# Optimization experiments

Hardware: AMD Instinct MI355X
Metric: run time of the kernel (lower is better)

Reference implementation:

```python
import jax, jax.numpy as jnp
import numpy as np

B, C, HH, WW = 8, 512, 32, 32
HEADS, GROUPS, EPS = 8, 32, 1e-5


def setup_inputs() -> dict:
    key = jax.random.key(0)
    k0, k1, k2 = jax.random.split(key, 3)
    x = jax.random.normal(k0, (B, C, HH, WW), jnp.float32)
    gamma = jnp.ones((C,), jnp.float32)
    beta = jnp.zeros((C,), jnp.float32)
    # 1x1 convs modeled as (out, in) matrices; fan-in scaling keeps logits sane
    w_qkv = jax.random.normal(k1, (3 * C, C), jnp.float32) * (C ** -0.5)
    b_qkv = jnp.zeros((3 * C,), jnp.float32)
    w_proj = jax.random.normal(k2, (C, C), jnp.float32) * (C ** -0.5)
    b_proj = jnp.zeros((C,), jnp.float32)
    return {"x": x, "gamma": gamma, "beta": beta, "w_qkv": w_qkv,
            "b_qkv": b_qkv, "w_proj": w_proj, "b_proj": b_proj}


def reference(x, gamma, beta, w_qkv, b_qkv, w_proj, b_proj):
    b, c, h, w = x.shape
    S = h * w
    xr = x.reshape(b, c, S)
    # GroupNorm(32, C) over (channels_in_group, spatial)
    xg = xr.reshape(b, GROUPS, c // GROUPS, S)
    mu = xg.mean(axis=(2, 3), keepdims=True)
    var = xg.var(axis=(2, 3), keepdims=True)
    xn = ((xg - mu) * jax.lax.rsqrt(var + EPS)).reshape(b, c, S)
    xn = xn * gamma[None, :, None] + beta[None, :, None]
    # qkv 1x1 conv: (B, 3C, S)
    qkv = jnp.einsum('oc,bcs->bos', w_qkv, xn) + b_qkv[None, :, None]
    D = c // HEADS
    qkv = qkv.reshape(b, 3, HEADS, D, S)  # channel layout: (three, H, D)
    q = jnp.transpose(qkv[:, 0], (0, 1, 3, 2))  # (B, H, S, D)
    k = jnp.transpose(qkv[:, 1], (0, 1, 3, 2))
    v = jnp.transpose(qkv[:, 2], (0, 1, 3, 2))
    scale = 1.0 / float(np.sqrt(np.sqrt(D)))
    logits = jnp.einsum('bhtd,bhsd->bhts', q * scale, k * scale)  # (B,H,S,S)
    logits = logits - jnp.max(logits, axis=-1, keepdims=True)
    probs = jax.nn.softmax(logits, axis=-1)  # dropout p=0 (default)
    attn = jnp.einsum('bhts,bhsd->bhtd', probs, v)  # (B,H,S,D)
    hout = jnp.transpose(attn, (0, 1, 3, 2)).reshape(b, c, S)  # (B, H*D=C, S)
    hout = jnp.einsum('oc,bcs->bos', w_proj, hout) + b_proj[None, :, None]
    return (hout + xr).reshape(b, c, h, w)
```

## Files before the change

kernel.cpp:

```cpp
#include <hip/hip_runtime.h>
#include <hip/hip_bf16.h>

typedef __hip_bfloat16 bf16;
typedef unsigned short u16;
typedef __attribute__((ext_vector_type(8))) short bf16x8;
typedef __attribute__((ext_vector_type(4))) float f32x4;

static constexpr int Bn = 8;
static constexpr int C = 512;
static constexpr int S = 1024;
static constexpr int NH = 8;
static constexpr int HD = 64;
static constexpr int CPG = 16;
#define EPSV 1e-5f

__device__ __forceinline__ u16 f2bf(float f) {
    bf16 h = __float2bfloat16(f);
    return *reinterpret_cast<u16*>(&h);
}

__device__ __forceinline__ void async_copy16(const void* g, void* l) {
    __builtin_amdgcn_global_load_lds(
        (const __attribute__((address_space(1))) void*)g,
        (__attribute__((address_space(3))) void*)l, 16, 0, 0);
}

__global__ __launch_bounds__(256) void wconv(const float* __restrict__ w,
                                             u16* __restrict__ out) {
    int i = (blockIdx.x * 256 + threadIdx.x) * 4;
    float4 v = *reinterpret_cast<const float4*>(&w[i]);
    float sc = (i < 512 * 512) ? 0.125f : 1.f;
    u16 t[4] = {f2bf(v.x * sc), f2bf(v.y * sc), f2bf(v.z * sc), f2bf(v.w * sc)};
    *reinterpret_cast<uint2*>(&out[i]) = *reinterpret_cast<uint2*>(t);
}

__global__ __launch_bounds__(256) void gn_stats(const float* __restrict__ x,
                                                float* __restrict__ stats) {
    const int tid = threadIdx.x;
    const int bg = blockIdx.x;
    const size_t base = (size_t)bg * CPG * S;
    const int N = CPG * S;
    float sum = 0.f, sq = 0.f;
    for (int i = tid * 4; i < N; i += 1024) {
        float4 v = *reinterpret_cast<const float4*>(&x[base + i]);
        sum += v.x + v.y + v.z + v.w;
        sq += v.x * v.x + v.y * v.y + v.z * v.z + v.w * v.w;
    }
#pragma unroll
    for (int off = 32; off > 0; off >>= 1) {
        sum += __shfl_down(sum, off, 64);
        sq  += __shfl_down(sq,  off, 64);
    }
    __shared__ float s0[4], s1[4];
    if ((tid & 63) == 0) { s0[tid >> 6] = sum; s1[tid >> 6] = sq; }
    __syncthreads();
    if (tid == 0) {
        float a  = s0[0] + s0[1] + s0[2] + s0[3];
        float b2 = s1[0] + s1[1] + s1[2] + s1[3];
        float mu = a / (float)N;
        float var = fmaxf(b2 / (float)N - mu * mu, 0.f);
        stats[bg] = mu;
        stats[256 + bg] = rsqrtf(var + EPSV);
    }
}

__global__ __launch_bounds__(256) void gn_apply_t(const float* __restrict__ x,
                                                  const float* __restrict__ gamma,
                                                  const float* __restrict__ beta,
                                                  const float* __restrict__ stats,
                                                  u16* __restrict__ xnt) {
    const int b = blockIdx.z, c0 = blockIdx.y * 64, s0 = blockIdx.x * 64;
    const int tid = threadIdx.x;
    __shared__ u16 T[64 * 72];
    const float* xb = x + ((size_t)b * C + c0) * S;
#pragma unroll
    for (int i = 0; i < 4; ++i) {
        int ch = i * 256 + tid;
        int c = ch >> 4, seg = ch & 15;
        int cg = c0 + c;
        float mu = stats[b * 32 + (cg >> 4)];
        float rstd = stats[256 + b * 32 + (cg >> 4)];
        float ga = gamma[cg], be = beta[cg];
        float4 v = *reinterpret_cast<const float4*>(&xb[(size_t)c * S + s0 + seg * 4]);
        float vals[4] = {v.x, v.y, v.z, v.w};
#pragma unroll
        for (int j = 0; j < 4; ++j)
            T[(seg * 4 + j) * 72 + c] = f2bf((vals[j] - mu) * rstd * ga + be);
    }
    __syncthreads();
#pragma unroll
    for (int i = 0; i < 2; ++i) {
        int ch = i * 256 + tid;
        int r = ch >> 3, seg = ch & 7;
        uint4 val = *reinterpret_cast<const uint4*>(&T[r * 72 + seg * 8]);
        *reinterpret_cast<uint4*>(&xnt[(size_t)(b * S + s0 + r) * C + c0 + seg * 8]) = val;
    }
}

template <int MODE>
__global__ __launch_bounds__(256) void mfma_gemm(const float* __restrict__ Wf,
                                                 const u16* __restrict__ Wb,
                                                 const u16* __restrict__ Xt,
                                                 const float* __restrict__ bias,
                                                 const float* __restrict__ resid,
                                                 u16* __restrict__ qkvT,
                                                 u16* __restrict__ qkvV,
                                                 float* __restrict__ Yf) {
    const int K = 512;
    const int b = blockIdx.z, o0 = blockIdx.y * 128, s0 = blockIdx.x * 128;
    const int tid = threadIdx.x;
    const int lane = tid & 63, w = tid >> 6;
    const int quad = lane >> 4, l15 = lane & 15;
    const int wr = w >> 1, wc = w & 1;
    __shared__ u16 As[128 * 64];
    __shared__ u16 Bs[128 * 64];
    f32x4 acc[4][4] = {};
    const u16* Xb = Xt + (size_t)(b * S + s0) * K;
    for (int k0 = 0; k0 < K; k0 += 64) {
        if (MODE == 0) {
#pragma unroll
            for (int i = 0; i < 4; ++i) {
                int ci = w * 4 + i;
                int r = ci * 8 + (lane >> 3);
                int c = (lane & 7) ^ (r & 7);
                async_copy16(&Wb[(size_t)(o0 + r) * K + k0 + c * 8], &As[ci * 512]);
            }
        } else {
#pragma unroll
            for (int i = 0; i < 4; ++i) {
                int ch = i * 256 + tid;
                int r = ch >> 3, c = ch & 7;
                const float* src = &Wf[(size_t)(o0 + r) * K + k0 + c * 8];
                float4 v0 = *reinterpret_cast<const float4*>(src);
                float4 v1 = *reinterpret_cast<const float4*>(src + 4);
                u16 tmp[8] = {f2bf(v0.x), f2bf(v0.y), f2bf(v0.z), f2bf(v0.w),
                              f2bf(v1.x), f2bf(v1.y), f2bf(v1.z), f2bf(v1.w)};
                *reinterpret_cast<uint4*>(&As[r * 64 + ((c ^ (r & 7)) << 3)]) =
                    *reinterpret_cast<uint4*>(tmp);
            }
        }
#pragma unroll
        for (int i = 0; i < 4; ++i) {
            int ci = w * 4 + i;
            int r = ci * 8 + (lane >> 3);
            int c = (lane & 7) ^ (r & 7);
            async_copy16(&Xb[(size_t)r * K + k0 + c * 8], &Bs[ci * 512]);
        }
        __syncthreads();
#pragma unroll
        for (int kk = 0; kk < 2; ++kk) {
            bf16x8 af[4], bfr[4];
#pragma unroll
            for (int mt = 0; mt < 4; ++mt) {
                int R = wr * 64 + mt * 16 + l15;
                af[mt] = *reinterpret_cast<const bf16x8*>(
                    &As[R * 64 + (((kk * 4 + quad) ^ (R & 7)) << 3)]);
            }
#pragma unroll
            for (int nt = 0; nt < 4; ++nt) {
                int R = wc * 64 + nt * 16 + l15;
                bfr[nt] = *reinterpret_cast<const bf16x8*>(
                    &Bs[R * 64 + (((kk * 4 + quad) ^ (R & 7)) << 3)]);
            }
#pragma unroll
            for (int mt = 0; mt < 4; ++mt)
#pragma unroll
                for (int nt = 0; nt < 4; ++nt)
                    acc[mt][nt] = __builtin_amdgcn_mfma_f32_16x16x32_bf16(
                        af[mt], bfr[nt], acc[mt][nt], 0, 0, 0);
        }
        __syncthreads();
    }
    if (MODE == 1) {
#pragma unroll
        for (int mt = 0; mt < 4; ++mt) {
#pragma unroll
            for (int reg = 0; reg < 4; ++reg) {
                int o = o0 + wr * 64 + mt * 16 + quad * 4 + reg;
                float bz = bias[o];
#pragma unroll
                for (int nt = 0; nt < 4; ++nt) {
                    int s = s0 + wc * 64 + nt * 16 + l15;
                    size_t idx = (size_t)(b * C + o) * S + s;
                    Yf[idx] = acc[mt][nt][reg] + bz + resid[idx];
                }
            }
        }
    } else if (o0 < 1024) {
        float bsc = (o0 < 512) ? 0.125f : 1.f;
#pragma unroll
        for (int mt = 0; mt < 4; ++mt) {
            int o_b = o0 + wr * 64 + mt * 16 + quad * 4;
            float bz[4];
#pragma unroll
            for (int reg = 0; reg < 4; ++reg) bz[reg] = bias[o_b + reg] * bsc;
#pragma unroll
            for (int nt = 0; nt < 4; ++nt) {
                int s = s0 + wc * 64 + nt * 16 + l15;
                u16 t4[4];
#pragma unroll
                for (int reg = 0; reg < 4; ++reg)
                    t4[reg] = f2bf(acc[mt][nt][reg] + bz[reg]);
                *reinterpret_cast<uint2*>(&qkvT[(size_t)(b * S + s) * 1024 + o_b]) =
                    *reinterpret_cast<uint2*>(t4);
            }
        }
    } else {
#pragma unroll
        for (int mt = 0; mt < 4; ++mt) {
#pragma unroll
            for (int reg = 0; reg < 4; ++reg) {
                int o = o0 - 1024 + wr * 64 + mt * 16 + quad * 4 + reg;
                float bz = bias[o + 1024];
#pragma unroll
                for (int nt = 0; nt < 4; ++nt) {
                    int s = s0 + wc * 64 + nt * 16 + l15;
                    qkvV[(size_t)(b * 512 + o) * S + s] = f2bf(acc[mt][nt][reg] + bz);
                }
            }
        }
    }
}

__global__ __launch_bounds__(256) void attn_mfma(const u16* __restrict__ qkvT,
                                                 const u16* __restrict__ qkvV,
                                                 u16* __restrict__ houtt) {
    const int b = blockIdx.z, h = blockIdx.y, q0 = blockIdx.x * 64;
    const int tid = threadIdx.x;
    const int lane = tid & 63, w = tid >> 6;
    const int quad = lane >> 4, l15 = lane & 15;
    __shared__ u16 qs[64 * 64];
    __shared__ u16 ks[64 * 64];
    __shared__ u16 vs[64 * 64];
    __shared__ u16 ps[64 * 72];

    const u16* qrow = qkvT + (size_t)(b * S + q0) * 1024 + h * HD;
#pragma unroll
    for (int i = 0; i < 2; ++i) {
        int ci = w * 2 + i;
        int r = ci * 8 + (lane >> 3);
        int c = (lane & 7) ^ (r & 7);
        async_copy16(&qrow[(size_t)r * 1024 + c * 8], &qs[ci * 512]);
    }
    __syncthreads();
    const int Rq = w * 16 + l15;
    bf16x8 qfrag[2];
#pragma unroll
    for (int kk = 0; kk < 2; ++kk)
        qfrag[kk] = *reinterpret_cast<const bf16x8*>(
            &qs[Rq * 64 + (((kk * 4 + quad) ^ (Rq & 7)) << 3)]);

    f32x4 o_acc[4] = {};
    float m_i = -INFINITY, l_i = 0.f;

    const u16* krow = qkvT + (size_t)b * S * 1024 + 512 + h * HD;
    const u16* vrow = qkvV + (size_t)(b * 512 + h * HD) * S;
    for (int kt = 0; kt < S; kt += 64) {
#pragma unroll
        for (int i = 0; i < 2; ++i) {
            int ci = w * 2 + i;
            int r = ci * 8 + (lane >> 3);
            int c = (lane & 7) ^ (r & 7);
            async_copy16(&krow[(size_t)(kt + r) * 1024 + c * 8], &ks[ci * 512]);
            async_copy16(&vrow[(size_t)r * S + kt + c * 8], &vs[ci * 512]);
        }
        __syncthreads();
        f32x4 s_acc[4] = {};
#pragma unroll
        for (int kk = 0; kk < 2; ++kk)
#pragma unroll
            for (int mt = 0; mt < 4; ++mt) {
                int Rk = mt * 16 + l15;
                bf16x8 kf = *reinterpret_cast<const bf16x8*>(
                    &ks[Rk * 64 + (((kk * 4 + quad) ^ (Rk & 7)) << 3)]);
                s_acc[mt] = __builtin_amdgcn_mfma_f32_16x16x32_bf16(
                    kf, qfrag[kk], s_acc[mt], 0, 0, 0);
            }
        float mx = -INFINITY;
#pragma unroll
        for (int mt = 0; mt < 4; ++mt)
#pragma unroll
            for (int reg = 0; reg < 4; ++reg) mx = fmaxf(mx, s_acc[mt][reg]);
        mx = fmaxf(mx, __shfl_xor(mx, 16, 64));
        mx = fmaxf(mx, __shfl_xor(mx, 32, 64));
        float mn = fmaxf(m_i, mx);
        float alpha = __expf(m_i - mn);
        float rs = 0.f;
#pragma unroll
        for (int mt = 0; mt < 4; ++mt)
#pragma unroll
            for (int reg = 0; reg < 4; ++reg) {
                float p = __expf(s_acc[mt][reg] - mn);
                s_acc[mt][reg] = p;
                rs += p;
            }
        rs += __shfl_xor(rs, 16, 64);
        rs += __shfl_xor(rs, 32, 64);
        l_i = l_i * alpha + rs;
        m_i = mn;
#pragma unroll
        for (int mt = 0; mt < 4; ++mt)
#pragma unroll
            for (int reg = 0; reg < 4; ++reg) o_acc[mt][reg] *= alpha;
#pragma unroll
        for (int mt = 0; mt < 4; ++mt) {
            u16 t4[4];
#pragma unroll
            for (int reg = 0; reg < 4; ++reg) t4[reg] = f2bf(s_acc[mt][reg]);
            *reinterpret_cast<uint2*>(&ps[Rq * 72 + mt * 16 + quad * 4]) =
                *reinterpret_cast<uint2*>(t4);
        }
#pragma unroll
        for (int kk = 0; kk < 2; ++kk) {
            bf16x8 pf = *reinterpret_cast<const bf16x8*>(
                &ps[Rq * 72 + kk * 32 + quad * 8]);
#pragma unroll
            for (int mt = 0; mt < 4; ++mt) {
                int Rv = mt * 16 + l15;
                bf16x8 vf = *reinterpret_cast<const bf16x8*>(
                    &vs[Rv * 64 + (((kk * 4 + quad) ^ (Rv & 7)) << 3)]);
                o_acc[mt] = __builtin_amdgcn_mfma_f32_16x16x32_bf16(
                    vf, pf, o_acc[mt], 0, 0, 0);
            }
        }
        __syncthreads();
    }
    float inv = 1.f / l_i;
    u16* orow = houtt + (size_t)(b * S + q0 + w * 16 + l15) * 512 + h * HD;
#pragma unroll
    for (int mt = 0; mt < 4; ++mt) {
        u16 t4[4];
#pragma unroll
        for (int reg = 0; reg < 4; ++reg) t4[reg] = f2bf(o_acc[mt][reg] * inv);
        *reinterpret_cast<uint2*>(&orow[mt * 16 + quad * 4]) =
            *reinterpret_cast<uint2*>(t4);
    }
}

extern "C" void kernel_launch(void* const* d_in, const int* in_sizes, int n_in,
                              void* d_out, int out_size, void* d_ws, size_t ws_size,
                              hipStream_t stream) {
    const float* x      = (const float*)d_in[0];
    const float* gamma  = (const float*)d_in[1];
    const float* beta   = (const float*)d_in[2];
    const float* w_qkv  = (const float*)d_in[3];
    const float* b_qkv  = (const float*)d_in[4];
    const float* w_proj = (const float*)d_in[5];
    const float* b_proj = (const float*)d_in[6];
    float* out = (float*)d_out;

    char* ws = (char*)d_ws;
    float* stats = (float*)ws;
    u16* wbf   = (u16*)(ws + 4096);
    u16* xnt   = (u16*)(ws + 4096 + 1572864);
    u16* qkvT  = (u16*)(ws + 4096 + 1572864 + 8388608);
    u16* qkvV  = (u16*)(ws + 4096 + 1572864 + 8388608 + 16777216);
    u16* houtt = xnt;

    wconv<<<768, 256, 0, stream>>>(w_qkv, wbf);
    gn_stats<<<Bn * 32, 256, 0, stream>>>(x, stats);
    gn_apply_t<<<dim3(16, 8, Bn), 256, 0, stream>>>(x, gamma, beta, stats, xnt);
    mfma_gemm<0><<<dim3(8, 12, Bn), 256, 0, stream>>>(
        nullptr, wbf, xnt, b_qkv, nullptr, qkvT, qkvV, nullptr);
    attn_mfma<<<dim3(16, NH, Bn), 256, 0, stream>>>(qkvT, qkvV, houtt);
    mfma_gemm<1><<<dim3(8, 4, Bn), 256, 0, stream>>>(
        w_proj, nullptr, houtt, b_proj, x, nullptr, nullptr, out);
}
```

Measured before the change: 170.5 us.

## Double-buffer attention K/V tiles, drop online max, prefold weight conversions

```diff
diff --git a/kernel.cpp b/kernel.cpp
--- a/kernel.cpp
+++ b/kernel.cpp
@@ -13,10 +13,15 @@
 static constexpr int HD = 64;
 static constexpr int CPG = 16;
 #define EPSV 1e-5f
+#define QSCALE 0.18033688011112042f
 
 __device__ __forceinline__ u16 f2bf(float f) {
     bf16 h = __float2bfloat16(f);
     return *reinterpret_cast<u16*>(&h);
+}
+__device__ __forceinline__ unsigned pack_bf2(float a, float b) {
+    __hip_bfloat162 h = __float22bfloat162_rn(make_float2(a, b));
+    return *reinterpret_cast<unsigned*>(&h);
 }
 
 __device__ __forceinline__ void async_copy16(const void* g, void* l) {
@@ -25,42 +30,50 @@
         (__attribute__((address_space(3))) void*)l, 16, 0, 0);
 }
 
-__global__ __launch_bounds__(256) void wconv(const float* __restrict__ w,
-                                             u16* __restrict__ out) {
-    int i = (blockIdx.x * 256 + threadIdx.x) * 4;
-    float4 v = *reinterpret_cast<const float4*>(&w[i]);
-    float sc = (i < 512 * 512) ? 0.125f : 1.f;
-    u16 t[4] = {f2bf(v.x * sc), f2bf(v.y * sc), f2bf(v.z * sc), f2bf(v.w * sc)};
-    *reinterpret_cast<uint2*>(&out[i]) = *reinterpret_cast<uint2*>(t);
-}
-
-__global__ __launch_bounds__(256) void gn_stats(const float* __restrict__ x,
-                                                float* __restrict__ stats) {
+__global__ __launch_bounds__(256) void prep(const float* __restrict__ x,
+                                            const float* __restrict__ wqkv,
+                                            const float* __restrict__ wproj,
+                                            float* __restrict__ stats,
+                                            u16* __restrict__ wbf) {
     const int tid = threadIdx.x;
-    const int bg = blockIdx.x;
-    const size_t base = (size_t)bg * CPG * S;
-    const int N = CPG * S;
-    float sum = 0.f, sq = 0.f;
-    for (int i = tid * 4; i < N; i += 1024) {
-        float4 v = *reinterpret_cast<const float4*>(&x[base + i]);
-        sum += v.x + v.y + v.z + v.w;
-        sq += v.x * v.x + v.y * v.y + v.z * v.z + v.w * v.w;
-    }
-#pragma unroll
-    for (int off = 32; off > 0; off >>= 1) {
-        sum += __shfl_down(sum, off, 64);
-        sq  += __shfl_down(sq,  off, 64);
-    }
-    __shared__ float s0[4], s1[4];
-    if ((tid & 63) == 0) { s0[tid >> 6] = sum; s1[tid >> 6] = sq; }
-    __syncthreads();
-    if (tid == 0) {
-        float a  = s0[0] + s0[1] + s0[2] + s0[3];
-        float b2 = s1[0] + s1[1] + s1[2] + s1[3];
-        float mu = a / (float)N;
-        float var = fmaxf(b2 / (float)N - mu * mu, 0.f);
-        stats[bg] = mu;
-        stats[256 + bg] = rsqrtf(var + EPSV);
+    if (blockIdx.x < 256) {
+        const int bg = blockIdx.x;
+        const size_t base = (size_t)bg * CPG * S;
+        const int N = CPG * S;
+        float sum = 0.f, sq = 0.f;
+        for (int i = tid * 4; i < N; i += 1024) {
+            float4 v = *reinterpret_cast<const float4*>(&x[base + i]);
+            sum += v.x + v.y + v.z + v.w;
+            sq += v.x * v.x + v.y * v.y + v.z * v.z + v.w * v.w;
+        }
+#pragma unroll
+        for (int off = 32; off > 0; off >>= 1) {
+            sum += __shfl_down(sum, off, 64);
+            sq  += __shfl_down(sq,  off, 64);
+        }
+        __shared__ float s0[4], s1[4];
+        if ((tid & 63) == 0) { s0[tid >> 6] = sum; s1[tid >> 6] = sq; }
+        __syncthreads();
+        if (tid == 0) {
+            float a  = s0[0] + s0[1] + s0[2] + s0[3];
+            float b2 = s1[0] + s1[1] + s1[2] + s1[3];
+            float mu = a / (float)N;
+            float var = fmaxf(b2 / (float)N - mu * mu, 0.f);
+            stats[bg] = mu;
+            stats[256 + bg] = rsqrtf(var + EPSV);
+        }
+    } else {
+        int idx = (blockIdx.x - 256) * 1024 + tid * 4;
+        float4 v;
+        float sc = 1.f;
+        if (idx < 1536 * 512) {
+            v = *reinterpret_cast<const float4*>(&wqkv[idx]);
+            if (idx < 512 * 512) sc = QSCALE;
+        } else {
+            v = *reinterpret_cast<const float4*>(&wproj[idx - 1536 * 512]);
+        }
+        u16 t[4] = {f2bf(v.x * sc), f2bf(v.y * sc), f2bf(v.z * sc), f2bf(v.w * sc)};
+        *reinterpret_cast<uint2*>(&wbf[idx]) = *reinterpret_cast<uint2*>(t);
     }
 }
 
@@ -98,8 +111,7 @@
 }
 
 template <int MODE>
-__global__ __launch_bounds__(256) void mfma_gemm(const float* __restrict__ Wf,
-                                                 const u16* __restrict__ Wb,
+__global__ __launch_bounds__(256) void mfma_gemm(const u16* __restrict__ Wb,
                                                  const u16* __restrict__ Xt,
                                                  const float* __restrict__ bias,
                                                  const float* __restrict__ resid,
@@ -117,33 +129,12 @@
     f32x4 acc[4][4] = {};
     const u16* Xb = Xt + (size_t)(b * S + s0) * K;
     for (int k0 = 0; k0 < K; k0 += 64) {
-        if (MODE == 0) {
-#pragma unroll
-            for (int i = 0; i < 4; ++i) {
-                int ci = w * 4 + i;
-                int r = ci * 8 + (lane >> 3);
-                int c = (lane & 7) ^ (r & 7);
-                async_copy16(&Wb[(size_t)(o0 + r) * K + k0 + c * 8], &As[ci * 512]);
-            }
-        } else {
-#pragma unroll
-            for (int i = 0; i < 4; ++i) {
-                int ch = i * 256 + tid;
-                int r = ch >> 3, c = ch & 7;
-                const float* src = &Wf[(size_t)(o0 + r) * K + k0 + c * 8];
-                float4 v0 = *reinterpret_cast<const float4*>(src);
-                float4 v1 = *reinterpret_cast<const float4*>(src + 4);
-                u16 tmp[8] = {f2bf(v0.x), f2bf(v0.y), f2bf(v0.z), f2bf(v0.w),
-                              f2bf(v1.x), f2bf(v1.y), f2bf(v1.z), f2bf(v1.w)};
-                *reinterpret_cast<uint4*>(&As[r * 64 + ((c ^ (r & 7)) << 3)]) =
-                    *reinterpret_cast<uint4*>(tmp);
-            }
-        }
 #pragma unroll
         for (int i = 0; i < 4; ++i) {
             int ci = w * 4 + i;
             int r = ci * 8 + (lane >> 3);
             int c = (lane & 7) ^ (r & 7);
+            async_copy16(&Wb[(size_t)(o0 + r) * K + k0 + c * 8], &As[ci * 512]);
             async_copy16(&Xb[(size_t)r * K + k0 + c * 8], &Bs[ci * 512]);
         }
         __syncthreads();
@@ -187,7 +178,7 @@
             }
         }
     } else if (o0 < 1024) {
-        float bsc = (o0 < 512) ? 0.125f : 1.f;
+        float bsc = (o0 < 512) ? QSCALE : 1.f;
 #pragma unroll
         for (int mt = 0; mt < 4; ++mt) {
             int o_b = o0 + wr * 64 + mt * 16 + quad * 4;
@@ -197,12 +188,10 @@
 #pragma unroll
             for (int nt = 0; nt < 4; ++nt) {
                 int s = s0 + wc * 64 + nt * 16 + l15;
-                u16 t4[4];
-#pragma unroll
-                for (int reg = 0; reg < 4; ++reg)
-                    t4[reg] = f2bf(acc[mt][nt][reg] + bz[reg]);
-                *reinterpret_cast<uint2*>(&qkvT[(size_t)(b * S + s) * 1024 + o_b]) =
-                    *reinterpret_cast<uint2*>(t4);
+                uint2 pk;
+                pk.x = pack_bf2(acc[mt][nt][0] + bz[0], acc[mt][nt][1] + bz[1]);
+                pk.y = pack_bf2(acc[mt][nt][2] + bz[2], acc[mt][nt][3] + bz[3]);
+                *reinterpret_cast<uint2*>(&qkvT[(size_t)(b * S + s) * 1024 + o_b]) = pk;
             }
         }
     } else {
@@ -230,17 +219,22 @@
     const int lane = tid & 63, w = tid >> 6;
     const int quad = lane >> 4, l15 = lane & 15;
     __shared__ u16 qs[64 * 64];
-    __shared__ u16 ks[64 * 64];
-    __shared__ u16 vs[64 * 64];
+    __shared__ u16 ks[2][64 * 64];
+    __shared__ u16 vs[2][64 * 64];
     __shared__ u16 ps[64 * 72];
 
     const u16* qrow = qkvT + (size_t)(b * S + q0) * 1024 + h * HD;
+    const u16* krow = qkvT + (size_t)b * S * 1024 + 512 + h * HD;
+    const u16* vrow = qkvV + (size_t)(b * 512 + h * HD) * S;
+
 #pragma unroll
     for (int i = 0; i < 2; ++i) {
         int ci = w * 2 + i;
         int r = ci * 8 + (lane >> 3);
         int c = (lane & 7) ^ (r & 7);
         async_copy16(&qrow[(size_t)r * 1024 + c * 8], &qs[ci * 512]);
+        async_copy16(&krow[(size_t)r * 1024 + c * 8], &ks[0][ci * 512]);
+        async_copy16(&vrow[(size_t)r * S + c * 8], &vs[0][ci * 512]);
     }
     __syncthreads();
     const int Rq = w * 16 + l15;
@@ -251,20 +245,21 @@
             &qs[Rq * 64 + (((kk * 4 + quad) ^ (Rq & 7)) << 3)]);
 
     f32x4 o_acc[4] = {};
-    float m_i = -INFINITY, l_i = 0.f;
-
-    const u16* krow = qkvT + (size_t)b * S * 1024 + 512 + h * HD;
-    const u16* vrow = qkvV + (size_t)(b * 512 + h * HD) * S;
-    for (int kt = 0; kt < S; kt += 64) {
-#pragma unroll
-        for (int i = 0; i < 2; ++i) {
-            int ci = w * 2 + i;
-            int r = ci * 8 + (lane >> 3);
-            int c = (lane & 7) ^ (r & 7);
-            async_copy16(&krow[(size_t)(kt + r) * 1024 + c * 8], &ks[ci * 512]);
-            async_copy16(&vrow[(size_t)r * S + kt + c * 8], &vs[ci * 512]);
-        }
-        __syncthreads();
+    float l_i = 0.f;
+
+    for (int t = 0; t < 16; ++t) {
+        const int cur = t & 1, nxt = cur ^ 1;
+        if (t < 15) {
+            int kt = (t + 1) * 64;
+#pragma unroll
+            for (int i = 0; i < 2; ++i) {
+                int ci = w * 2 + i;
+                int r = ci * 8 + (lane >> 3);
+                int c = (lane & 7) ^ (r & 7);
+                async_copy16(&krow[(size_t)(kt + r) * 1024 + c * 8], &ks[nxt][ci * 512]);
+                async_copy16(&vrow[(size_t)r * S + kt + c * 8], &vs[nxt][ci * 512]);
+            }
+        }
         f32x4 s_acc[4] = {};
 #pragma unroll
         for (int kk = 0; kk < 2; ++kk)
@@ -272,44 +267,24 @@
             for (int mt = 0; mt < 4; ++mt) {
                 int Rk = mt * 16 + l15;
                 bf16x8 kf = *reinterpret_cast<const bf16x8*>(
-                    &ks[Rk * 64 + (((kk * 4 + quad) ^ (Rk & 7)) << 3)]);
+                    &ks[cur][Rk * 64 + (((kk * 4 + quad) ^ (Rk & 7)) << 3)]);
                 s_acc[mt] = __builtin_amdgcn_mfma_f32_16x16x32_bf16(
                     kf, qfrag[kk], s_acc[mt], 0, 0, 0);
             }
-        float mx = -INFINITY;
-#pragma unroll
-        for (int mt = 0; mt < 4; ++mt)
-#pragma unroll
-            for (int reg = 0; reg < 4; ++reg) mx = fmaxf(mx, s_acc[mt][reg]);
-        mx = fmaxf(mx, __shfl_xor(mx, 16, 64));
-        mx = fmaxf(mx, __shfl_xor(mx, 32, 64));
-        float mn = fmaxf(m_i, mx);
-        float alpha = __expf(m_i - mn);
         float rs = 0.f;
 #pragma unroll
-        for (int mt = 0; mt < 4; ++mt)
-#pragma unroll
-            for (int reg = 0; reg < 4; ++reg) {
-                float p = __expf(s_acc[mt][reg] - mn);
-                s_acc[mt][reg] = p;
-                rs += p;
-            }
-        rs += __shfl_xor(rs, 16, 64);
-        rs += __shfl_xor(rs, 32, 64);
-        l_i = l_i * alpha + rs;
-        m_i = mn;
-#pragma unroll
-        for (int mt = 0; mt < 4; ++mt)
-#pragma unroll
-            for (int reg = 0; reg < 4; ++reg) o_acc[mt][reg] *= alpha;
-#pragma unroll
         for (int mt = 0; mt < 4; ++mt) {
-            u16 t4[4];
-#pragma unroll
-            for (int reg = 0; reg < 4; ++reg) t4[reg] = f2bf(s_acc[mt][reg]);
-            *reinterpret_cast<uint2*>(&ps[Rq * 72 + mt * 16 + quad * 4]) =
-                *reinterpret_cast<uint2*>(t4);
-        }
+            float p0 = __builtin_amdgcn_exp2f(s_acc[mt][0]);
+            float p1 = __builtin_amdgcn_exp2f(s_acc[mt][1]);
+            float p2 = __builtin_amdgcn_exp2f(s_acc[mt][2]);
+            float p3 = __builtin_amdgcn_exp2f(s_acc[mt][3]);
+            rs += (p0 + p1) + (p2 + p3);
+            uint2 pk;
+            pk.x = pack_bf2(p0, p1);
+            pk.y = pack_bf2(p2, p3);
+            *reinterpret_cast<uint2*>(&ps[Rq * 72 + mt * 16 + quad * 4]) = pk;
+        }
+        l_i += rs;
 #pragma unroll
         for (int kk = 0; kk < 2; ++kk) {
             bf16x8 pf = *reinterpret_cast<const bf16x8*>(
@@ -318,22 +293,23 @@
             for (int mt = 0; mt < 4; ++mt) {
                 int Rv = mt * 16 + l15;
                 bf16x8 vf = *reinterpret_cast<const bf16x8*>(
-                    &vs[Rv * 64 + (((kk * 4 + quad) ^ (Rv & 7)) << 3)]);
+                    &vs[cur][Rv * 64 + (((kk * 4 + quad) ^ (Rv & 7)) << 3)]);
                 o_acc[mt] = __builtin_amdgcn_mfma_f32_16x16x32_bf16(
                     vf, pf, o_acc[mt], 0, 0, 0);
             }
         }
         __syncthreads();
     }
+    l_i += __shfl_xor(l_i, 16, 64);
+    l_i += __shfl_xor(l_i, 32, 64);
     float inv = 1.f / l_i;
     u16* orow = houtt + (size_t)(b * S + q0 + w * 16 + l15) * 512 + h * HD;
 #pragma unroll
     for (int mt = 0; mt < 4; ++mt) {
-        u16 t4[4];
-#pragma unroll
-        for (int reg = 0; reg < 4; ++reg) t4[reg] = f2bf(o_acc[mt][reg] * inv);
-        *reinterpret_cast<uint2*>(&orow[mt * 16 + quad * 4]) =
-            *reinterpret_cast<uint2*>(t4);
+        uint2 pk;
+        pk.x = pack_bf2(o_acc[mt][0] * inv, o_acc[mt][1] * inv);
+        pk.y = pack_bf2(o_acc[mt][2] * inv, o_acc[mt][3] * inv);
+        *reinterpret_cast<uint2*>(&orow[mt * 16 + quad * 4]) = pk;
     }
 }
 
@@ -352,17 +328,16 @@
     char* ws = (char*)d_ws;
     float* stats = (float*)ws;
     u16* wbf   = (u16*)(ws + 4096);
-    u16* xnt   = (u16*)(ws + 4096 + 1572864);
-    u16* qkvT  = (u16*)(ws + 4096 + 1572864 + 8388608);
-    u16* qkvV  = (u16*)(ws + 4096 + 1572864 + 8388608 + 16777216);
+    u16* xnt   = (u16*)(ws + 4096 + 2097152);
+    u16* qkvT  = (u16*)(ws + 4096 + 2097152 + 8388608);
+    u16* qkvV  = (u16*)(ws + 4096 + 2097152 + 8388608 + 16777216);
     u16* houtt = xnt;
 
-    wconv<<<768, 256, 0, stream>>>(w_qkv, wbf);
-    gn_stats<<<Bn * 32, 256, 0, stream>>>(x, stats);
+    prep<<<1280, 256, 0, stream>>>(x, w_qkv, w_proj, stats, wbf);
     gn_apply_t<<<dim3(16, 8, Bn), 256, 0, stream>>>(x, gamma, beta, stats, xnt);
     mfma_gemm<0><<<dim3(8, 12, Bn), 256, 0, stream>>>(
-        nullptr, wbf, xnt, b_qkv, nullptr, qkvT, qkvV, nullptr);
+        wbf, xnt, b_qkv, nullptr, qkvT, qkvV, nullptr);
     attn_mfma<<<dim3(16, NH, Bn), 256, 0, stream>>>(qkvT, qkvV, houtt);
     mfma_gemm<1><<<dim3(8, 4, Bn), 256, 0, stream>>>(
-        w_proj, nullptr, houtt, b_proj, x, nullptr, nullptr, out);
-}
+        wbf + 1536 * 512, houtt, b_proj, x, nullptr, nullptr, out);
+}
```

New measurement: 172.6 us. About the same (+1.2%).
